# Kernel optimization log

Measured on AMD Instinct MI355X. Metric: run time of the kernel, lower is better.

Reference implementation:

```python
import jax, jax.numpy as jnp
import numpy as np

N_NODES = 260000          # 10,000 graphs * 26 nodes/graph (split size hardcoded in Net)
N_EDGES = 8320000         # avg degree 32
GRAPH_NODES = 26
IN_DIM, H1, H2 = 4, 26, 11
POOL_OUT = 4              # MaxPool1d(3, stride=3, padding=1) on 11 channels -> 4


def setup_inputs() -> dict:
    key = jax.random.key(0)
    ks = jax.random.split(key, 8)
    x = jax.random.normal(ks[0], (N_NODES, IN_DIM), dtype=jnp.float32)
    edge_index = jax.random.randint(ks[1], (2, N_EDGES), 0, N_NODES, dtype=jnp.int32)
    W1 = jax.random.normal(ks[2], (H1, IN_DIM), dtype=jnp.float32) * 0.3
    b1 = jax.random.normal(ks[3], (H1,), dtype=jnp.float32) * 0.1
    W2 = jax.random.normal(ks[4], (H2, H1), dtype=jnp.float32) * 0.2
    b2 = jax.random.normal(ks[5], (H2,), dtype=jnp.float32) * 0.1
    Wl = jax.random.normal(ks[6], (2, POOL_OUT), dtype=jnp.float32) * 0.3
    bl = jax.random.normal(ks[7], (2,), dtype=jnp.float32) * 0.1
    return {"x": x, "edge_index": edge_index, "W1": W1, "b1": b1,
            "W2": W2, "b2": b2, "Wl": Wl, "bl": bl}


def reference(x, edge_index, W1, b1, W2, b2, Wl, bl):
    N = x.shape[0]
    # add_self_loops
    loops = jnp.arange(N, dtype=edge_index.dtype)
    row = jnp.concatenate([edge_index[0], loops])
    col = jnp.concatenate([edge_index[1], loops])

    def gcn(h, W, b):
        h = h @ W.T + b                       # Linear
        # message: deg = ones -> norm = 1, so message is just x_j = h[row]
        # aggr='add': scatter-add into target nodes (col)
        return jax.ops.segment_sum(h[row], col, num_segments=N)

    h = jnp.tanh(gcn(x, W1, b1))              # [N, 26]
    h = jnp.tanh(gcn(h, W2, b2))              # [N, 11]

    # MaxPool1d(kernel=3, stride=3, padding=1) over the 11 channels -> 4.
    # Left pad by 1 with -inf; the right pad element is never inside a window.
    neg = jnp.full((N, 1), -jnp.inf, dtype=h.dtype)
    hp = jnp.concatenate([neg, h], axis=1)    # [N, 12]
    pooled = hp.reshape(N, POOL_OUT, 3).max(axis=2)  # [N, 4]

    # graph pooling: sum every consecutive block of 26 nodes
    g = pooled.reshape(-1, GRAPH_NODES, POOL_OUT).sum(axis=1)  # [G, 4]

    out = g @ Wl.T + bl                        # [G, 2]
    return jax.nn.softmax(out, axis=-1)        # F.softmax default dim=1 for 2D
```

## Files before the change

### kernel.cpp

```cpp
#include <hip/hip_runtime.h>
#include <hip/hip_fp16.h>

#define N_NODES 260000
#define N_EDGES 8320000
#define H1 26
#define H2 11
#define GRAPH_NODES 26
#define N_GRAPHS 10000

#define NB 128
#define NBUCK 2032
#define NPB 256
#define PBT 1024
#define EPB 32500
#define ZS 16
#define FSTRIDE 13
#define EREG 24

#define TB1 86668u
#define TB2 173336u

#define NTL(p) __builtin_nontemporal_load(p)

typedef unsigned int u32x4 __attribute__((ext_vector_type(4)));
typedef unsigned int u32x2 __attribute__((ext_vector_type(2)));

__device__ __forceinline__ float2 up2(unsigned u) {
    __half2 h = *reinterpret_cast<const __half2*>(&u);
    return __half22float2(h);
}
__device__ __forceinline__ unsigned pk2(float a, float b) {
    __half2 h = __floats2half2_rn(a, b);
    return *reinterpret_cast<const unsigned*>(&h);
}

__global__ __launch_bounds__(256) void zero_kernel(unsigned* __restrict__ ghist,
                                                   float* __restrict__ gpool) {
    int i = blockIdx.x * 256 + threadIdx.x;
    if (i < NBUCK) ghist[i] = 0u;
    if (i < N_GRAPHS * 4) gpool[i] = 0.f;
}

__global__ __launch_bounds__(PBT) void count_kernel(const int* __restrict__ col,
                                                    unsigned* __restrict__ ghist) {
    __shared__ unsigned lh[NBUCK];
    for (int b = threadIdx.x; b < NBUCK; b += PBT) lh[b] = 0u;
    __syncthreads();
    int e0 = blockIdx.x * EPB, e1 = e0 + EPB;
    for (int e = e0 + threadIdx.x; e < e1; e += PBT)
        atomicAdd(&lh[((unsigned)NTL(&col[e])) >> 7], 1u);
    __syncthreads();
    for (int b = threadIdx.x; b < NBUCK; b += PBT)
        if (lh[b]) atomicAdd(&ghist[b], lh[b]);
}

__global__ __launch_bounds__(1024) void scan_kernel(const unsigned* __restrict__ ghist,
                                                    unsigned* __restrict__ bstart,
                                                    unsigned* __restrict__ bfill) {
    __shared__ unsigned v[2048];
    int t = threadIdx.x;
    int t1 = t + 1024;
    v[t]  = (t  < NBUCK) ? ghist[t]  : 0u;
    v[t1] = (t1 < NBUCK) ? ghist[t1] : 0u;
    __syncthreads();
    for (int off = 1; off < 2048; off <<= 1) {
        unsigned a0 = (t  >= off) ? v[t  - off] : 0u;
        unsigned a1 = (t1 >= off) ? v[t1 - off] : 0u;
        __syncthreads();
        v[t]  += a0;
        v[t1] += a1;
        __syncthreads();
    }
    if (t < NBUCK) {
        unsigned st = (t == 0) ? 0u : v[t - 1];
        bstart[t] = st; bfill[t] = st;
    }
    if (t1 < NBUCK) {
        unsigned st = v[t1 - 1];
        bstart[t1] = st; bfill[t1] = st;
        if (t1 == NBUCK - 1) bstart[NBUCK] = v[t1];
    }
}

__global__ __launch_bounds__(PBT) void place_kernel(const int* __restrict__ row,
                                                    const int* __restrict__ col,
                                                    unsigned* __restrict__ bfill,
                                                    unsigned* __restrict__ part) {
    __shared__ unsigned lh[NBUCK];
    __shared__ unsigned lbase[NBUCK];
    for (int b = threadIdx.x; b < NBUCK; b += PBT) lh[b] = 0u;
    __syncthreads();
    int e0 = blockIdx.x * EPB, e1 = e0 + EPB;
    for (int e = e0 + threadIdx.x; e < e1; e += PBT)
        atomicAdd(&lh[((unsigned)NTL(&col[e])) >> 7], 1u);
    __syncthreads();
    for (int b = threadIdx.x; b < NBUCK; b += PBT) {
        unsigned c = lh[b];
        lbase[b] = c ? atomicAdd(&bfill[b], c) : 0u;
    }
    __syncthreads();
    for (int b = threadIdx.x; b < NBUCK; b += PBT) lh[b] = 0u;
    __syncthreads();
    for (int e = e0 + threadIdx.x; e < e1; e += PBT) {
        unsigned c = (unsigned)NTL(&col[e]);
        unsigned r = (unsigned)NTL(&row[e]);
        unsigned b = c >> 7;
        unsigned p = lbase[b] + atomicAdd(&lh[b], 1u);
        __builtin_nontemporal_store((r << 7) | (c & 127u), &part[p]);
    }
}

__device__ __forceinline__ void acc_node(float* acc, unsigned cl, float4 xv) {
    float* a = acc + cl * 5;
    atomicAdd(&a[0], xv.x); atomicAdd(&a[1], xv.y);
    atomicAdd(&a[2], xv.z); atomicAdd(&a[3], xv.w);
    atomicAdd(&a[4], 1.f);
}

__global__ __launch_bounds__(256) void layer1_kernel(const unsigned* __restrict__ part,
                                                     const unsigned* __restrict__ bstart,
                                                     const float* __restrict__ x,
                                                     const float* __restrict__ W1,
                                                     const float* __restrict__ b1,
                                                     const float* __restrict__ W2,
                                                     const float* __restrict__ b2,
                                                     ushort* __restrict__ zmsg) {
    __shared__ float acc[NB * 5];
    __shared__ float sW1[H1 * 4], sb1[H1], sW2[H2 * H1];
    for (int t = threadIdx.x; t < H1 * 4; t += 256) sW1[t] = W1[t];
    for (int t = threadIdx.x; t < H1; t += 256) sb1[t] = b1[t];
    for (int t = threadIdx.x; t < H2 * H1; t += 256) sW2[t] = W2[t];
    for (int t = threadIdx.x; t < NB * 5; t += 256) acc[t] = 0.f;
    __syncthreads();
    unsigned s = bstart[blockIdx.x], e = bstart[blockIdx.x + 1];
    unsigned i = s + threadIdx.x;
    for (; i + 256 < e; i += 512) {
        unsigned u1 = NTL(&part[i]), u2 = NTL(&part[i + 256]);
        unsigned r1 = u1 >> 7, cl1 = u1 & 127u;
        unsigned r2 = u2 >> 7, cl2 = u2 & 127u;
        float4 x1 = ((const float4*)x)[r1];
        float4 x2 = ((const float4*)x)[r2];
        acc_node(acc, cl1, x1);
        acc_node(acc, cl2, x2);
    }
    if (i < e) {
        unsigned u = NTL(&part[i]);
        acc_node(acc, u & 127u, ((const float4*)x)[u >> 7]);
    }
    __syncthreads();
    int base = blockIdx.x * NB;
    for (int n = threadIdx.x; n < NB; n += 256) {
        int node = base + n;
        if (node >= N_NODES) continue;
        float4 xv = ((const float4*)x)[node];
        float sx = acc[n*5+0] + xv.x, sy = acc[n*5+1] + xv.y;
        float sz = acc[n*5+2] + xv.z, sw = acc[n*5+3] + xv.w;
        float deg = acc[n*5+4] + 1.f;
        float h[H1];
        #pragma unroll
        for (int j = 0; j < H1; ++j)
            h[j] = tanhf(sb1[j] * deg + sx * sW1[j*4+0] + sy * sW1[j*4+1]
                                      + sz * sW1[j*4+2] + sw * sW1[j*4+3]);
        float z[H2];
        #pragma unroll
        for (int jj = 0; jj < H2; ++jj) {
            float v = 0.f;
            #pragma unroll
            for (int k = 0; k < H1; ++k) v += h[k] * sW2[jj*H1 + k];
            z[jj] = v;
        }
        u32x4 lo;
        u32x2 hi;
        lo.x = pk2(z[0], z[1]);  lo.y = pk2(z[2], z[3]);
        lo.z = pk2(z[4], z[5]);  lo.w = pk2(z[6], z[7]);
        hi.x = pk2(z[8], z[9]);  hi.y = pk2(z[10], deg);
        ushort* zp = zmsg + (size_t)node * ZS;
        __builtin_nontemporal_store(lo, (u32x4*)zp);
        __builtin_nontemporal_store(hi, (u32x2*)(zp + 8));
    }
}

__device__ __forceinline__ void acc_edge(float* facc, unsigned cl, u32x4 A, u32x2 B) {
    float* f = facc + cl * FSTRIDE;
    float2 v;
    v = up2(A.x); atomicAdd(&f[0], v.x); atomicAdd(&f[1], v.y);
    v = up2(A.y); atomicAdd(&f[2], v.x); atomicAdd(&f[3], v.y);
    v = up2(A.z); atomicAdd(&f[4], v.x); atomicAdd(&f[5], v.y);
    v = up2(A.w); atomicAdd(&f[6], v.x); atomicAdd(&f[7], v.y);
    v = up2(B.x); atomicAdd(&f[8], v.x); atomicAdd(&f[9], v.y);
    v = up2(B.y); atomicAdd(&f[10], v.x);
}

__global__ __launch_bounds__(256) void layer2_kernel(const unsigned* __restrict__ part,
                                                     const unsigned* __restrict__ bstart,
                                                     const ushort* __restrict__ zmsg,
                                                     const float* __restrict__ b2,
                                                     float* __restrict__ gpool) {
    __shared__ float facc[NB * FSTRIDE];
    __shared__ float sb2[H2];
    __shared__ float gacc[7][4];
    if (threadIdx.x < H2) sb2[threadIdx.x] = b2[threadIdx.x];
    if (threadIdx.x < 28) ((float*)gacc)[threadIdx.x] = 0.f;
    __syncthreads();
    int base = blockIdx.x * NB;
    for (int n = threadIdx.x; n < NB; n += 256) {
        const ushort* zp = zmsg + (size_t)(base + n) * ZS;
        u32x4 A = *(const u32x4*)zp;
        u32x2 B = *(const u32x2*)(zp + 8);
        float2 vd = up2(B.y);
        float deg = vd.y;
        float* f = facc + n * FSTRIDE;
        float2 v;
        v = up2(A.x); f[0] = v.x + deg*sb2[0]; f[1] = v.y + deg*sb2[1];
        v = up2(A.y); f[2] = v.x + deg*sb2[2]; f[3] = v.y + deg*sb2[3];
        v = up2(A.z); f[4] = v.x + deg*sb2[4]; f[5] = v.y + deg*sb2[5];
        v = up2(A.w); f[6] = v.x + deg*sb2[6]; f[7] = v.y + deg*sb2[7];
        v = up2(B.x); f[8] = v.x + deg*sb2[8]; f[9] = v.y + deg*sb2[9];
        f[10] = vd.x + deg*sb2[10];
    }
    __syncthreads();
    unsigned s = bstart[blockIdx.x], e = bstart[blockIdx.x + 1];
    unsigned ed[EREG];
    #pragma unroll
    for (int k = 0; k < EREG; ++k) {
        unsigned idx = s + threadIdx.x + (unsigned)k * 256u;
        ed[k] = (idx < e) ? NTL(&part[idx]) : 0xFFFFFFFFu;
    }
    const unsigned lob[4] = {0u, TB1, TB2, (unsigned)N_NODES};
    #pragma unroll
    for (int ps = 0; ps < 3; ++ps) {
        unsigned lo = lob[ps], hi = lob[ps + 1];
        #pragma unroll
        for (int k = 0; k < EREG; ++k) {
            unsigned u = ed[k];
            unsigned r = u >> 7;
            if (r >= lo && r < hi) {
                unsigned cl = u & 127u;
                const ushort* p = zmsg + (size_t)r * ZS;
                u32x4 A = *(const u32x4*)p;
                u32x2 B = *(const u32x2*)(p + 8);
                acc_edge(facc, cl, A, B);
            }
        }
    }
    for (unsigned i = s + threadIdx.x + EREG * 256u; i < e; i += 256u) {
        unsigned u = part[i];
        unsigned r = u >> 7, cl = u & 127u;
        const ushort* p = zmsg + (size_t)r * ZS;
        u32x4 A = *(const u32x4*)p;
        u32x2 B = *(const u32x2*)(p + 8);
        acc_edge(facc, cl, A, B);
    }
    __syncthreads();
    int gfirst = base / GRAPH_NODES;
    int lastnode = min(base + NB - 1, N_NODES - 1);
    int glast = lastnode / GRAPH_NODES;
    for (int n = threadIdx.x; n < NB; n += 256) {
        int node = base + n;
        if (node >= N_NODES) continue;
        const float* h = facc + n * FSTRIDE;
        float p0 = tanhf(fmaxf(h[0], h[1]));
        float p1 = tanhf(fmaxf(fmaxf(h[2], h[3]), h[4]));
        float p2 = tanhf(fmaxf(fmaxf(h[5], h[6]), h[7]));
        float p3 = tanhf(fmaxf(fmaxf(h[8], h[9]), h[10]));
        int lg = node / GRAPH_NODES - gfirst;
        atomicAdd(&gacc[lg][0], p0);
        atomicAdd(&gacc[lg][1], p1);
        atomicAdd(&gacc[lg][2], p2);
        atomicAdd(&gacc[lg][3], p3);
    }
    __syncthreads();
    int ng = glast - gfirst + 1;
    for (int t = threadIdx.x; t < ng * 4; t += 256) {
        int lg = t >> 2, c = t & 3;
        float v = gacc[lg][c];
        if (v != 0.f) atomicAdd(&gpool[(size_t)(gfirst + lg) * 4 + c], v);
    }
}

__global__ __launch_bounds__(256) void final_kernel(const float* __restrict__ gpool,
                                                    const float* __restrict__ Wl,
                                                    const float* __restrict__ bl,
                                                    float* __restrict__ out) {
    int g = blockIdx.x * 256 + threadIdx.x;
    if (g >= N_GRAPHS) return;
    float4 p = ((const float4*)gpool)[g];
    float o0 = bl[0] + p.x * Wl[0] + p.y * Wl[1] + p.z * Wl[2] + p.w * Wl[3];
    float o1 = bl[1] + p.x * Wl[4] + p.y * Wl[5] + p.z * Wl[6] + p.w * Wl[7];
    float m = fmaxf(o0, o1);
    float e0 = expf(o0 - m), e1 = expf(o1 - m);
    float s = e0 + e1;
    out[g * 2 + 0] = e0 / s;
    out[g * 2 + 1] = e1 / s;
}

extern "C" void kernel_launch(void* const* d_in, const int* in_sizes, int n_in,
                              void* d_out, int out_size, void* d_ws, size_t ws_size,
                              hipStream_t stream) {
    const float* x  = (const float*)d_in[0];
    const int* ei   = (const int*)d_in[1];
    const float* W1 = (const float*)d_in[2];
    const float* b1 = (const float*)d_in[3];
    const float* W2 = (const float*)d_in[4];
    const float* b2 = (const float*)d_in[5];
    const float* Wl = (const float*)d_in[6];
    const float* bl = (const float*)d_in[7];
    float* out = (float*)d_out;

    const int* row = ei;
    const int* col = ei + N_EDGES;

    ushort*   zmsg   = (ushort*)d_ws;
    unsigned* part   = (unsigned*)((char*)d_ws + (size_t)NBUCK * NB * ZS * 2);
    unsigned* bstart = part + N_EDGES;
    unsigned* bfill  = bstart + NBUCK + 1;
    unsigned* ghist  = bfill + NBUCK;
    float*    gpool  = (float*)(ghist + NBUCK);

    zero_kernel<<<(N_GRAPHS*4 + 255)/256, 256, 0, stream>>>(ghist, gpool);
    count_kernel<<<NPB, PBT, 0, stream>>>(col, ghist);
    scan_kernel<<<1, 1024, 0, stream>>>(ghist, bstart, bfill);
    place_kernel<<<NPB, PBT, 0, stream>>>(row, col, bfill, part);
    layer1_kernel<<<NBUCK, 256, 0, stream>>>(part, bstart, x, W1, b1, W2, b2, zmsg);
    layer2_kernel<<<NBUCK, 256, 0, stream>>>(part, bstart, zmsg, b2, gpool);
    final_kernel<<<(N_GRAPHS + 255)/256, 256, 0, stream>>>(gpool, Wl, bl, out);
}
```

Before: 1.153 ms.

## Batch eight gathers per iteration in both layers, drop range-partitioned passes

```diff
diff --git a/kernel.cpp b/kernel.cpp
--- a/kernel.cpp
+++ b/kernel.cpp
@@ -15,10 +15,6 @@
 #define EPB 32500
 #define ZS 16
 #define FSTRIDE 13
-#define EREG 24
-
-#define TB1 86668u
-#define TB2 173336u
 
 #define NTL(p) __builtin_nontemporal_load(p)
 
@@ -134,16 +130,18 @@
     __syncthreads();
     unsigned s = bstart[blockIdx.x], e = bstart[blockIdx.x + 1];
     unsigned i = s + threadIdx.x;
-    for (; i + 256 < e; i += 512) {
-        unsigned u1 = NTL(&part[i]), u2 = NTL(&part[i + 256]);
-        unsigned r1 = u1 >> 7, cl1 = u1 & 127u;
-        unsigned r2 = u2 >> 7, cl2 = u2 & 127u;
-        float4 x1 = ((const float4*)x)[r1];
-        float4 x2 = ((const float4*)x)[r2];
-        acc_node(acc, cl1, x1);
-        acc_node(acc, cl2, x2);
-    }
-    if (i < e) {
+    while (i + 7u * 256u < e) {
+        unsigned us[8];
+        float4 xs[8];
+        #pragma unroll
+        for (int j = 0; j < 8; ++j) us[j] = NTL(&part[i + (unsigned)j * 256u]);
+        #pragma unroll
+        for (int j = 0; j < 8; ++j) xs[j] = ((const float4*)x)[us[j] >> 7];
+        #pragma unroll
+        for (int j = 0; j < 8; ++j) acc_node(acc, us[j] & 127u, xs[j]);
+        i += 8u * 256u;
+    }
+    for (; i < e; i += 256u) {
         unsigned u = NTL(&part[i]);
         acc_node(acc, u & 127u, ((const float4*)x)[u >> 7]);
     }
@@ -220,36 +218,29 @@
     }
     __syncthreads();
     unsigned s = bstart[blockIdx.x], e = bstart[blockIdx.x + 1];
-    unsigned ed[EREG];
-    #pragma unroll
-    for (int k = 0; k < EREG; ++k) {
-        unsigned idx = s + threadIdx.x + (unsigned)k * 256u;
-        ed[k] = (idx < e) ? NTL(&part[idx]) : 0xFFFFFFFFu;
-    }
-    const unsigned lob[4] = {0u, TB1, TB2, (unsigned)N_NODES};
-    #pragma unroll
-    for (int ps = 0; ps < 3; ++ps) {
-        unsigned lo = lob[ps], hi = lob[ps + 1];
-        #pragma unroll
-        for (int k = 0; k < EREG; ++k) {
-            unsigned u = ed[k];
-            unsigned r = u >> 7;
-            if (r >= lo && r < hi) {
-                unsigned cl = u & 127u;
-                const ushort* p = zmsg + (size_t)r * ZS;
-                u32x4 A = *(const u32x4*)p;
-                u32x2 B = *(const u32x2*)(p + 8);
-                acc_edge(facc, cl, A, B);
-            }
+    unsigned i = s + threadIdx.x;
+    while (i + 7u * 256u < e) {
+        unsigned us[8];
+        u32x4 A[8];
+        u32x2 B[8];
+        #pragma unroll
+        for (int j = 0; j < 8; ++j) us[j] = NTL(&part[i + (unsigned)j * 256u]);
+        #pragma unroll
+        for (int j = 0; j < 8; ++j) {
+            const ushort* p = zmsg + (size_t)(us[j] >> 7) * ZS;
+            A[j] = *(const u32x4*)p;
+            B[j] = *(const u32x2*)(p + 8);
         }
-    }
-    for (unsigned i = s + threadIdx.x + EREG * 256u; i < e; i += 256u) {
-        unsigned u = part[i];
-        unsigned r = u >> 7, cl = u & 127u;
-        const ushort* p = zmsg + (size_t)r * ZS;
+        #pragma unroll
+        for (int j = 0; j < 8; ++j) acc_edge(facc, us[j] & 127u, A[j], B[j]);
+        i += 8u * 256u;
+    }
+    for (; i < e; i += 256u) {
+        unsigned u = NTL(&part[i]);
+        const ushort* p = zmsg + (size_t)(u >> 7) * ZS;
         u32x4 A = *(const u32x4*)p;
         u32x2 B = *(const u32x2*)(p + 8);
-        acc_edge(facc, cl, A, B);
+        acc_edge(facc, u & 127u, A, B);
     }
     __syncthreads();
     int gfirst = base / GRAPH_NODES;
```

Measured after the change: 1.168 ms. No clear change (+1.3%).
